# Kernel tuning notes

Measured on AMD Instinct MI355X. Metric: run time of the kernel, lower is better.

Reference implementation:

```python
import jax, jax.numpy as jnp
import numpy as np

N_NODES = 100000
N_EDGES = 600000
D = 128  # input_dim == output_dim (required by index_add into zeros_like(x) + residual)
EPS = 1e-5


def _linear_params(key, d_in, d_out):
    kw, kb = jax.random.split(key)
    bound = 1.0 / np.sqrt(d_in)
    w = jax.random.uniform(kw, (d_in, d_out), minval=-bound, maxval=bound, dtype=jnp.float32)
    b = jax.random.uniform(kb, (d_out,), minval=-bound, maxval=bound, dtype=jnp.float32)
    return w, b


def setup_inputs() -> dict:
    key = jax.random.key(0)
    ks = jax.random.split(key, 6)
    x = jax.random.normal(ks[0], (N_NODES, D), dtype=jnp.float32)
    edge_index = jax.random.randint(ks[1], (2, N_EDGES), 0, N_NODES, dtype=jnp.int32)
    w_m1, b_m1 = _linear_params(ks[2], 2 * D, D)
    w_m2, b_m2 = _linear_params(ks[3], D, D)
    w_u1, b_u1 = _linear_params(ks[4], 2 * D, D)
    w_u2, b_u2 = _linear_params(ks[5], D, D)
    gamma = jnp.ones((D,), dtype=jnp.float32)
    beta = jnp.zeros((D,), dtype=jnp.float32)
    return {
        "x": x, "edge_index": edge_index,
        "w_m1": w_m1, "b_m1": b_m1, "w_m2": w_m2, "b_m2": b_m2,
        "w_u1": w_u1, "b_u1": b_u1, "w_u2": w_u2, "b_u2": b_u2,
        "gamma": gamma, "beta": beta,
    }


def _layernorm(h, gamma, beta):
    mu = jnp.mean(h, axis=-1, keepdims=True)
    var = jnp.mean(jnp.square(h - mu), axis=-1, keepdims=True)
    return (h - mu) * jax.lax.rsqrt(var + EPS) * gamma + beta


def reference(x, edge_index, w_m1, b_m1, w_m2, b_m2, w_u1, b_u1, w_u2, b_u2, gamma, beta):
    row, col = edge_index[0], edge_index[1]
    # message MLP on concat of gathered endpoints: [E, 2D] -> [E, D]
    m_in = jnp.concatenate([x[row], x[col]], axis=-1)
    m = jax.nn.relu(m_in @ w_m1 + b_m1) @ w_m2 + b_m2
    # scatter-add messages to destination nodes (index_add along dim 0 with col)
    agg = jax.ops.segment_sum(m, col, num_segments=x.shape[0])
    # update MLP on [N, 2D] -> [N, D]
    u_in = jnp.concatenate([x, agg], axis=-1)
    h = jax.nn.relu(u_in @ w_u1 + b_u1) @ w_u2 + b_u2
    return _layernorm(h, gamma, beta) + x
```

## Files before the change

kernel.cpp:

```cpp
#include <hip/hip_runtime.h>
#include <hip/hip_bf16.h>
#include <stdint.h>

#define N_NODES 100000
#define N_EDGES 600000
#define D 128
#define EPS 1e-5f
#define SCAN_BS 512
#define ROW_MASK 0x1FFFF

#define PREP_BLOCKS 321
#define HIST_BLOCKS 2344
#define XF_BLOCKS   3125
#define SC_BLOCKS   2344
#define UPD_BLOCKS  3125

typedef __attribute__((ext_vector_type(8))) short short8;
typedef __attribute__((ext_vector_type(16))) float floatx16;


__device__ __forceinline__ uint32_t pack_bf16_rne(float lo, float hi) {
    uint32_t ul = __builtin_bit_cast(uint32_t, lo);
    uint32_t uh = __builtin_bit_cast(uint32_t, hi);
    ul += 0x7fffu + ((ul >> 16) & 1u);
    uh += 0x7fffu + ((uh >> 16) & 1u);
    return (ul >> 16) | (uh & 0xffff0000u);
}

__device__ __forceinline__ unsigned short f32_to_bf16_rne(float f) {
    uint32_t u = __builtin_bit_cast(uint32_t, f);
    u += 0x7fffu + ((u >> 16) & 1u);
    return (unsigned short)(u >> 16);
}

__device__ __forceinline__ float bflo(uint32_t a) { return __builtin_bit_cast(float, a << 16); }
__device__ __forceinline__ float bfhi(uint32_t a) { return __builtin_bit_cast(float, a & 0xffff0000u); }

__global__ void prep_hist(const float* __restrict__ w_m1, const float* __restrict__ w_u1,
                          const float* __restrict__ w_u2, const float* __restrict__ w_m2,
                          const float* __restrict__ b_m2,
                          unsigned short* __restrict__ wm1f, unsigned short* __restrict__ wu1tf,
                          unsigned short* __restrict__ wu2f, unsigned short* __restrict__ wcf,
                          float* __restrict__ vb,
                          const int* __restrict__ col, int* __restrict__ count,
                          int* __restrict__ rank) {
    if (blockIdx.x >= PREP_BLOCKS) {
        int e = (blockIdx.x - PREP_BLOCKS) * 256 + threadIdx.x;
        if (e < N_EDGES) rank[e] = atomicAdd(&count[col[e]], 1);
        return;
    }
    int idx = blockIdx.x * 256 + threadIdx.x;
    if (idx < 32768) {
        int j = idx & 7, lane = (idx >> 3) & 63, t = (idx >> 9) & 3, s = idx >> 11;
        int kk = s * 16 + ((lane >> 5) << 3) + j;
        wm1f[idx] = f32_to_bf16_rne(w_m1[kk * 128 + t * 32 + (lane & 31)]);
    } else if (idx < 49152) {
        int ii = idx - 32768;
        int j = ii & 7, lane = (ii >> 3) & 63, t = (ii >> 9) & 3, s = ii >> 11;
        int kk = s * 16 + ((lane >> 5) << 3) + j;
        wu1tf[ii] = f32_to_bf16_rne(w_u1[kk * 128 + t * 32 + (lane & 31)]);
    } else if (idx < 65536) {
        int ii = idx - 49152;
        int j = ii & 7, lane = (ii >> 3) & 63, t = (ii >> 9) & 3, s = ii >> 11;
        int kk = s * 16 + ((lane >> 5) << 3) + j;
        wu2f[ii] = f32_to_bf16_rne(w_u2[kk * 128 + t * 32 + (lane & 31)]);
    } else if (idx < 81920) {
        int ii = idx - 65536;
        int j = ii & 7, lane = (ii >> 3) & 63, t = (ii >> 9) & 3, s = ii >> 11;
        int kk = s * 16 + ((lane >> 5) << 3) + j;
        int nn = t * 32 + (lane & 31);
        float acc = 0.0f;
        for (int q = 0; q < 128; ++q)
            acc += w_m2[kk * 128 + q] * w_u1[(128 + q) * 128 + nn];
        wcf[ii] = f32_to_bf16_rne(acc);
    } else if (idx < 82048) {
        int nn = idx - 81920;
        float acc = 0.0f;
        for (int q = 0; q < 128; ++q)
            acc += b_m2[q] * w_u1[(128 + q) * 128 + nn];
        vb[nn] = acc;
    }
}

__global__ void scan_one(const int* __restrict__ count, int* __restrict__ base,
                         int* __restrict__ gcur) {
    __shared__ int tmp[SCAN_BS];
    __shared__ int bbase;
    int g = blockIdx.x * SCAN_BS + threadIdx.x;
    int v = (g < N_NODES) ? count[g] : 0;
    tmp[threadIdx.x] = v;
    __syncthreads();
    int acc = v;
#pragma unroll
    for (int off = 1; off < SCAN_BS; off <<= 1) {
        int add = (threadIdx.x >= off) ? tmp[threadIdx.x - off] : 0;
        __syncthreads();
        acc += add;
        tmp[threadIdx.x] = acc;
        __syncthreads();
    }
    if (threadIdx.x == SCAN_BS - 1) bbase = atomicAdd(gcur, acc);
    __syncthreads();
    if (g < N_NODES) base[g] = bbase + acc - v;
}

__launch_bounds__(64, 4)
__global__ void xform_scatter(const float* __restrict__ x, const short8* __restrict__ w1f,
                              const float* __restrict__ b1, unsigned short* __restrict__ xtb,
                              const int* __restrict__ row, const int* __restrict__ col,
                              const int* __restrict__ rank, const int* __restrict__ base,
                              int* __restrict__ srow) {
    if (blockIdx.x >= XF_BLOCKS) {
        int e4 = (((blockIdx.x - XF_BLOCKS) * 64 + threadIdx.x) << 2);
        if (e4 < N_EDGES) {
            int4 r4 = *(const int4*)(row + e4);
            int4 c4 = *(const int4*)(col + e4);
            int4 k4 = *(const int4*)(rank + e4);
            srow[base[c4.x] + k4.x] = r4.x | ((c4.x & 31) << 17);
            srow[base[c4.y] + k4.y] = r4.y | ((c4.y & 31) << 17);
            srow[base[c4.z] + k4.z] = r4.z | ((c4.z & 31) << 17);
            srow[base[c4.w] + k4.w] = r4.w | ((c4.w & 31) << 17);
        }
        return;
    }

    __shared__ __align__(16) short h1[32 * 136];
    const int lane = threadIdx.x;
    const int l31  = lane & 31;
    const int half = lane >> 5;
    short* hl = h1;

    const int nbase = blockIdx.x * 32;
    const int n = nbase + l31;
    const float* px = x + (size_t)n * D + half * 8;

    union { short8 v; uint32_t u[4]; } fa[8];
#pragma unroll
    for (int s = 0; s < 8; ++s) {
        const int off = s * 16;
        float4 a0 = *(const float4*)(px + off);
        float4 a1 = *(const float4*)(px + off + 4);
        fa[s].u[0] = pack_bf16_rne(a0.x, a0.y); fa[s].u[1] = pack_bf16_rne(a0.z, a0.w);
        fa[s].u[2] = pack_bf16_rne(a1.x, a1.y); fa[s].u[3] = pack_bf16_rne(a1.z, a1.w);
    }

#pragma unroll
    for (int p = 0; p < 2; ++p) {
        floatx16 acc[4];
#pragma unroll
        for (int t = 0; t < 4; ++t) acc[t] = (floatx16)0.0f;
#pragma unroll
        for (int s = 0; s < 8; ++s) {
#pragma unroll
            for (int t = 0; t < 4; ++t) {
                short8 wf = w1f[((p * 8 + s) * 4 + t) * 64 + lane];
                acc[t] = __builtin_amdgcn_mfma_f32_32x32x16_bf16(fa[s].v, wf, acc[t], 0, 0, 0);
            }
        }
#pragma unroll
        for (int t = 0; t < 4; ++t) {
            float bias = p ? b1[t * 32 + l31] : 0.0f;
#pragma unroll
            for (int r = 0; r < 16; ++r) {
                int m = (r & 3) + 8 * (r >> 2) + 4 * half;
                hl[m * 136 + t * 32 + l31] = (short)f32_to_bf16_rne(acc[t][r] + bias);
            }
        }
#pragma unroll
        for (int it = 0; it < 8; ++it) {
            int off = it * 512 + lane * 8;
            int r2 = off >> 7;
            int c2 = off & 127;
            short8 v = *(const short8*)(hl + r2 * 136 + c2);
            *(short8*)(xtb + (size_t)(nbase + r2) * 256 + p * 128 + c2) = v;
        }
    }
}

__launch_bounds__(64, 2)
__global__ void upd_kernel(const float* __restrict__ x, const uint32_t* __restrict__ xtb32,
                           const int* __restrict__ srowpk,
                           const int* __restrict__ base, const int* __restrict__ count,
                           const short8* __restrict__ wu1tf, const short8* __restrict__ wcf,
                           const short8* __restrict__ wu2f,
                           const float* __restrict__ b_u1, const float* __restrict__ vb,
                           const float* __restrict__ b_u2,
                           const float* __restrict__ gamma, const float* __restrict__ beta,
                           float* __restrict__ out) {
    __shared__ __align__(16) short h1[32 * 136];
    __shared__ __align__(16) uint32_t XBlds[32 * 64];
    const int lane = threadIdx.x;
    const int l31  = lane & 31;
    const int half = lane >> 5;
    const int t    = lane & 15;
    const int q16  = lane & 48;
    short* hl = h1;
    uint32_t* accu = (uint32_t*)hl;

    const int nbase = blockIdx.x * 32;
    const int nc = nbase + l31;

    const int b_l = base[nc];
    const int c_l = count[nc];
    const float dgv = (float)c_l;

    const int qsrc = q16 >> 1;
    const int qbeg = __shfl(b_l, qsrc);
    const int qend = __shfl(b_l, qsrc + 7) + __shfl(c_l, qsrc + 7);

    int ncm = (qend - qbeg + 15) >> 4;
    ncm = max(ncm, __shfl_xor(ncm, 16));
    ncm = max(ncm, __shfl_xor(ncm, 32));

#pragma unroll
    for (int i = 0; i < 8; ++i) {
        uint4 z; z.x = 0; z.y = 0; z.z = 0; z.w = 0;
        *((uint4*)accu + i * 64 + lane) = z;
    }

#pragma unroll
    for (int j = 0; j < 8; ++j) {
        int fi = j * 64 + lane;
        int i  = fi >> 4;
        int k  = fi & 15;
        uint4 v = *(const uint4*)(xtb32 + (size_t)(nbase + i) * 128 + 64 + (k << 2));
        *((uint4*)XBlds + fi) = v;
    }

    {
        float sl0 = 0.f, sl1 = 0.f, sl2 = 0.f, sl3 = 0.f;
        float sh0 = 0.f, sh1 = 0.f, sh2 = 0.f, sh3 = 0.f;
        int curnib = -1;

        auto flush = [&]() {
            uint4 o;
            o.x = pack_bf16_rne(sl0, sh0);
            o.y = pack_bf16_rne(sl1, sh1);
            o.z = pack_bf16_rne(sl2, sh2);
            o.w = pack_bf16_rne(sl3, sh3);
            *(uint4*)(accu + (curnib << 6) + (t << 2)) = o;
        };

        int pk = 0;
        { int idx = qbeg + t; if (idx < qend) pk = srowpk[idx]; }

        for (int c = 0; c < ncm; ++c) {
            const int rem = qend - qbeg - (c << 4);

            int pknext = 0;
            { int idx = qbeg + ((c + 1) << 4) + t; if (idx < qend) pknext = srowpk[idx]; }

            uint4 xt[16];
#pragma unroll
            for (int e = 0; e < 16; ++e) {
                int pv = __shfl(pk, q16 + e);
                uint4 z; z.x = 0; z.y = 0; z.z = 0; z.w = 0;
                xt[e] = z;
                if (e < rem)
                    xt[e] = *(const uint4*)(xtb32 + (size_t)(pv & ROW_MASK) * 128 + (t << 2));
            }

#pragma unroll
            for (int e = 0; e < 16; ++e) {
                int pv = __shfl(pk, q16 + e);
                if (e < rem) {
                    int nib = pv >> 17;
                    uint4 xb = *(const uint4*)(XBlds + (nib << 6) + (t << 2));
                    float a0 = fmaxf(bflo(xt[e].x) + bflo(xb.x), 0.f);
                    float b0 = fmaxf(bfhi(xt[e].x) + bfhi(xb.x), 0.f);
                    float a1 = fmaxf(bflo(xt[e].y) + bflo(xb.y), 0.f);
                    float b1 = fmaxf(bfhi(xt[e].y) + bfhi(xb.y), 0.f);
                    float a2 = fmaxf(bflo(xt[e].z) + bflo(xb.z), 0.f);
                    float b2 = fmaxf(bfhi(xt[e].z) + bfhi(xb.z), 0.f);
                    float a3 = fmaxf(bflo(xt[e].w) + bflo(xb.w), 0.f);
                    float b3 = fmaxf(bfhi(xt[e].w) + bfhi(xb.w), 0.f);
                    if (nib != curnib) {
                        if (curnib >= 0) flush();
                        curnib = nib;
                        sl0 = a0; sh0 = b0; sl1 = a1; sh1 = b1;
                        sl2 = a2; sh2 = b2; sl3 = a3; sh3 = b3;
                    } else {
                        sl0 += a0; sh0 += b0; sl1 += a1; sh1 += b1;
                        sl2 += a2; sh2 += b2; sl3 += a3; sh3 += b3;
                    }
                }
            }
            pk = pknext;
        }
        if (curnib >= 0) flush();
    }

    const float* px = x + (size_t)nc * D + half * 8;

    floatx16 acc[4];
#pragma unroll
    for (int tt = 0; tt < 4; ++tt) acc[tt] = (floatx16)0.0f;

#pragma unroll
    for (int s = 0; s < 16; ++s) {
        union { short8 v; uint32_t u[4]; } fa;
        const short8* bf;
        if (s < 8) {
            const int off = s * 16;
            float4 a0 = *(const float4*)(px + off);
            float4 a1 = *(const float4*)(px + off + 4);
            fa.u[0] = pack_bf16_rne(a0.x, a0.y); fa.u[1] = pack_bf16_rne(a0.z, a0.w);
            fa.u[2] = pack_bf16_rne(a1.x, a1.y); fa.u[3] = pack_bf16_rne(a1.z, a1.w);
            bf = wu1tf + (s * 4) * 64;
        } else {
            fa.v = *(const short8*)((const short*)accu + l31 * 128 + (s - 8) * 16 + half * 8);
            bf = wcf + ((s - 8) * 4) * 64;
        }
#pragma unroll
        for (int tt = 0; tt < 4; ++tt) {
            short8 wf = bf[tt * 64 + lane];
            acc[tt] = __builtin_amdgcn_mfma_f32_32x32x16_bf16(fa.v, wf, acc[tt], 0, 0, 0);
        }
    }

    float bu1[4], vbt[4];
#pragma unroll
    for (int tt = 0; tt < 4; ++tt) {
        bu1[tt] = b_u1[tt * 32 + l31];
        vbt[tt] = vb[tt * 32 + l31];
    }

#pragma unroll
    for (int r = 0; r < 16; ++r) {
        int m = (r & 3) + 8 * (r >> 2) + 4 * half;
        float dg = __shfl(dgv, m, 32);
#pragma unroll
        for (int tt = 0; tt < 4; ++tt) {
            float v = fmaxf(acc[tt][r] + bu1[tt] + dg * vbt[tt], 0.0f);
            hl[m * 136 + tt * 32 + l31] = (short)f32_to_bf16_rne(v);
        }
    }

    floatx16 acc2[4];
#pragma unroll
    for (int tt = 0; tt < 4; ++tt) acc2[tt] = (floatx16)0.0f;

#pragma unroll
    for (int s = 0; s < 8; ++s) {
        short8 af = *(const short8*)(hl + l31 * 136 + s * 16 + half * 8);
#pragma unroll
        for (int tt = 0; tt < 4; ++tt) {
            short8 wf = wu2f[(s * 4 + tt) * 64 + lane];
            acc2[tt] = __builtin_amdgcn_mfma_f32_32x32x16_bf16(af, wf, acc2[tt], 0, 0, 0);
        }
    }

    float g4[4], be4[4], bias2[4];
#pragma unroll
    for (int tt = 0; tt < 4; ++tt) {
        g4[tt]    = gamma[tt * 32 + l31];
        be4[tt]   = beta[tt * 32 + l31];
        bias2[tt] = b_u2[tt * 32 + l31];
    }

    float* hf = (float*)hl;
#pragma unroll
    for (int p = 0; p < 2; ++p) {
#pragma unroll
        for (int rr = 0; rr < 8; ++rr) {
            int r = p * 8 + rr;
            float hv[4];
            float s1 = 0.0f, s2 = 0.0f;
#pragma unroll
            for (int tt = 0; tt < 4; ++tt) {
                hv[tt] = acc2[tt][r] + bias2[tt];
                s1 += hv[tt];
                s2 += hv[tt] * hv[tt];
            }
#pragma unroll
            for (int mask = 1; mask < 32; mask <<= 1) {
                s1 += __shfl_xor(s1, mask);
                s2 += __shfl_xor(s2, mask);
            }
            float mean = s1 * (1.0f / 128.0f);
            float var  = s2 * (1.0f / 128.0f) - mean * mean;
            float rs   = rsqrtf(var + EPS);
            int m = (r & 3) + 8 * (r >> 2) + 4 * half;
            int mrow = m - 16 * p;
#pragma unroll
            for (int tt = 0; tt < 4; ++tt)
                hf[mrow * 132 + tt * 32 + l31] = (hv[tt] - mean) * rs * g4[tt] + be4[tt];
        }
#pragma unroll
        for (int it = 0; it < 8; ++it) {
            int qq = it * 64 + lane;
            int r2 = qq >> 5;
            int c4 = qq & 31;
            int node = nbase + 16 * p + r2;
            float4 v = *(const float4*)(hf + r2 * 132 + c4 * 4);
            float4 xr = *(const float4*)(x + (size_t)node * D + c4 * 4);
            v.x += xr.x; v.y += xr.y; v.z += xr.z; v.w += xr.w;
            *(float4*)(out + (size_t)node * D + c4 * 4) = v;
        }
    }
}

extern "C" void kernel_launch(void* const* d_in, const int* in_sizes, int n_in,
                              void* d_out, int out_size, void* d_ws, size_t ws_size,
                              hipStream_t stream) {
    const float* x     = (const float*)d_in[0];
    const int*   edge  = (const int*)d_in[1];
    const float* w_m1  = (const float*)d_in[2];
    const float* b_m1  = (const float*)d_in[3];
    const float* w_m2  = (const float*)d_in[4];
    const float* b_m2  = (const float*)d_in[5];
    const float* w_u1  = (const float*)d_in[6];
    const float* b_u1  = (const float*)d_in[7];
    const float* w_u2  = (const float*)d_in[8];
    const float* b_u2  = (const float*)d_in[9];
    const float* gamma = (const float*)d_in[10];
    const float* beta  = (const float*)d_in[11];
    float* out = (float*)d_out;

    char* ws = (char*)d_ws;
    size_t off = 0;
    auto alloc = [&](size_t bytes) { void* p = ws + off; off = (off + bytes + 15) & ~(size_t)15; return p; };

    unsigned short* xtb   = (unsigned short*)alloc((size_t)N_NODES * 256 * 2);
    unsigned short* wm1f  = (unsigned short*)alloc(256 * 128 * 2);
    unsigned short* wu1tf = (unsigned short*)alloc(128 * 128 * 2);
    unsigned short* wcf   = (unsigned short*)alloc(128 * 128 * 2);
    unsigned short* wu2f  = (unsigned short*)alloc(128 * 128 * 2);
    float* vb    = (float*)alloc(128 * 4);
    int* count   = (int*)alloc((size_t)N_NODES * 4 + 16);
    int* gcur    = count + N_NODES;
    int* base    = (int*)alloc((size_t)N_NODES * 4);
    int* rank    = (int*)alloc((size_t)N_EDGES * 4);
    int* srow    = (int*)alloc((size_t)N_EDGES * 4);

    const int* rowi = edge;
    const int* coli = edge + N_EDGES;
    const int NB = (N_NODES + SCAN_BS - 1) / SCAN_BS;

    (void)hipMemsetAsync(count, 0, (size_t)N_NODES * 4 + 16, stream);

    prep_hist<<<PREP_BLOCKS + HIST_BLOCKS, 256, 0, stream>>>(
        w_m1, w_u1, w_u2, w_m2, b_m2, wm1f, wu1tf, wu2f, wcf, vb, coli, count, rank);

    scan_one<<<NB, SCAN_BS, 0, stream>>>(count, base, gcur);

    xform_scatter<<<XF_BLOCKS + SC_BLOCKS, 64, 0, stream>>>(
        x, (const short8*)wm1f, b_m1, xtb, rowi, coli, rank, base, srow);

    upd_kernel<<<UPD_BLOCKS, 64, 0, stream>>>(
        x, (const uint32_t*)xtb, srow, base, count,
        (const short8*)wu1tf, (const short8*)wcf, (const short8*)wu2f,
        b_u1, vb, b_u2, gamma, beta, out);
}
```

Baseline: 256.3 us.

## Double-buffer edge-row gathers so loads overlap with the accumulate loop

Restructures the per-chunk gather loop into a two-stage software pipeline with A/B register buffers. The next chunk's 16 row loads are issued before the current chunk is consumed, and sched_barrier keeps the compiler from reordering them. Loads now happen unconditionally, with out-of-range entries clamped to row 0 and index reads clamped to N_EDGES-1, which removes the divergent guards. The aim is to hide global-memory gather latency behind compute, at the cost of roughly doubling the vector registers held for gathered rows, which may lower occupancy.

```diff
diff --git a/kernel.cpp b/kernel.cpp
--- a/kernel.cpp
+++ b/kernel.cpp
@@ -207,8 +207,9 @@
     const int qsrc = q16 >> 1;
     const int qbeg = __shfl(b_l, qsrc);
     const int qend = __shfl(b_l, qsrc + 7) + __shfl(c_l, qsrc + 7);
-
-    int ncm = (qend - qbeg + 15) >> 4;
+    const int rembase = qend - qbeg;
+
+    int ncm = (rembase + 15) >> 4;
     ncm = max(ncm, __shfl_xor(ncm, 16));
     ncm = max(ncm, __shfl_xor(ncm, 32));
 
@@ -241,30 +242,26 @@
             *(uint4*)(accu + (curnib << 6) + (t << 2)) = o;
         };
 
-        int pk = 0;
-        { int idx = qbeg + t; if (idx < qend) pk = srowpk[idx]; }
-
-        for (int c = 0; c < ncm; ++c) {
-            const int rem = qend - qbeg - (c << 4);
-
-            int pknext = 0;
-            { int idx = qbeg + ((c + 1) << 4) + t; if (idx < qend) pknext = srowpk[idx]; }
-
-            uint4 xt[16];
+        auto ldpk = [&](int c) -> int {
+            int idx = qbeg + (c << 4) + t;
+            return srowpk[min(idx, N_EDGES - 1)];
+        };
+
+        auto issue = [&](int pkv, int c, uint4* xt, int* pv) {
 #pragma unroll
             for (int e = 0; e < 16; ++e) {
-                int pv = __shfl(pk, q16 + e);
-                uint4 z; z.x = 0; z.y = 0; z.z = 0; z.w = 0;
-                xt[e] = z;
-                if (e < rem)
-                    xt[e] = *(const uint4*)(xtb32 + (size_t)(pv & ROW_MASK) * 128 + (t << 2));
-            }
-
+                int p = __shfl(pkv, q16 + e);
+                if ((c << 4) + e >= rembase) p = 0;
+                pv[e] = p;
+                xt[e] = *(const uint4*)(xtb32 + (size_t)(p & ROW_MASK) * 128 + (t << 2));
+            }
+        };
+
+        auto consume = [&](const uint4* xt, const int* pv, int rem) {
 #pragma unroll
             for (int e = 0; e < 16; ++e) {
-                int pv = __shfl(pk, q16 + e);
                 if (e < rem) {
-                    int nib = pv >> 17;
+                    int nib = pv[e] >> 17;
                     uint4 xb = *(const uint4*)(XBlds + (nib << 6) + (t << 2));
                     float a0 = fmaxf(bflo(xt[e].x) + bflo(xb.x), 0.f);
                     float b0 = fmaxf(bfhi(xt[e].x) + bfhi(xb.x), 0.f);
@@ -285,7 +282,25 @@
                     }
                 }
             }
-            pk = pknext;
+        };
+
+        uint4 xtA[16], xtB[16];
+        int pvA[16], pvB[16];
+
+        int pkc = ldpk(0);
+        issue(pkc, 0, xtA, pvA);
+        int pkn = ldpk(1);
+
+        for (int cc = 0; cc < ncm; cc += 2) {
+            issue(pkn, cc + 1, xtB, pvB);
+            pkc = ldpk(cc + 2);
+            __builtin_amdgcn_sched_barrier(0);
+            consume(xtA, pvA, rembase - (cc << 4));
+
+            issue(pkc, cc + 2, xtA, pvA);
+            pkn = ldpk(cc + 3);
+            __builtin_amdgcn_sched_barrier(0);
+            consume(xtB, pvB, rembase - ((cc + 1) << 4));
         }
         if (curnib >= 0) flush();
     }
```

After: 254.6 us. About the same (-0.7%).

## Pipeline edge-row gathers through LDS ring with async global_load_lds

Applied to the files above, without the earlier changes.

Replaces the register-held 16-edge gather batch in upd_kernel with a double-buffered LDS ring fed by global_load_lds, processing 4 edges per step and prefetching packed indices and gathered rows two steps ahead using manual vmcnt waits. It also raises launch bounds occupancy from 2 to 4 waves per SIMD hint. This aims to cut VGPR pressure and overlap gather latency with the accumulation work. The hand-tuned vmcnt counts are fragile, and smaller batches mean more loop iterations and synchronization overhead.

```diff
diff --git a/kernel.cpp b/kernel.cpp
--- a/kernel.cpp
+++ b/kernel.cpp
@@ -35,6 +35,17 @@
 
 __device__ __forceinline__ float bflo(uint32_t a) { return __builtin_bit_cast(float, a << 16); }
 __device__ __forceinline__ float bfhi(uint32_t a) { return __builtin_bit_cast(float, a & 0xffff0000u); }
+
+__device__ __forceinline__ void glds16(const void* g, void* l) {
+    __builtin_amdgcn_global_load_lds(
+        (const __attribute__((address_space(1))) void*)g,
+        (__attribute__((address_space(3))) void*)l, 16, 0, 0);
+}
+__device__ __forceinline__ void glds4(const void* g, void* l) {
+    __builtin_amdgcn_global_load_lds(
+        (const __attribute__((address_space(1))) void*)g,
+        (__attribute__((address_space(3))) void*)l, 4, 0, 0);
+}
 
 __global__ void prep_hist(const float* __restrict__ w_m1, const float* __restrict__ w_u1,
                           const float* __restrict__ w_u2, const float* __restrict__ w_m2,
@@ -177,7 +188,7 @@
     }
 }
 
-__launch_bounds__(64, 2)
+__launch_bounds__(64, 4)
 __global__ void upd_kernel(const float* __restrict__ x, const uint32_t* __restrict__ xtb32,
                            const int* __restrict__ srowpk,
                            const int* __restrict__ base, const int* __restrict__ count,
@@ -189,6 +200,8 @@
                            float* __restrict__ out) {
     __shared__ __align__(16) short h1[32 * 136];
     __shared__ __align__(16) uint32_t XBlds[32 * 64];
+    __shared__ __align__(16) uint32_t xtring[2048];
+    __shared__ __align__(16) uint32_t pkring[128];
     const int lane = threadIdx.x;
     const int l31  = lane & 31;
     const int half = lane >> 5;
@@ -207,8 +220,9 @@
     const int qsrc = q16 >> 1;
     const int qbeg = __shfl(b_l, qsrc);
     const int qend = __shfl(b_l, qsrc + 7) + __shfl(c_l, qsrc + 7);
-
-    int ncm = (qend - qbeg + 15) >> 4;
+    const int rembase = qend - qbeg;
+
+    int ncm = (rembase + 3) >> 2;
     ncm = max(ncm, __shfl_xor(ncm, 16));
     ncm = max(ncm, __shfl_xor(ncm, 32));
 
@@ -227,10 +241,11 @@
         *((uint4*)XBlds + fi) = v;
     }
 
-    {
+    if (ncm > 0) {
         float sl0 = 0.f, sl1 = 0.f, sl2 = 0.f, sl3 = 0.f;
         float sh0 = 0.f, sh1 = 0.f, sh2 = 0.f, sh3 = 0.f;
         int curnib = -1;
+        int pkcur = 0, pknext = 0;
 
         auto flush = [&]() {
             uint4 o;
@@ -241,39 +256,37 @@
             *(uint4*)(accu + (curnib << 6) + (t << 2)) = o;
         };
 
-        int pk = 0;
-        { int idx = qbeg + t; if (idx < qend) pk = srowpk[idx]; }
-
-        for (int c = 0; c < ncm; ++c) {
-            const int rem = qend - qbeg - (c << 4);
-
-            int pknext = 0;
-            { int idx = qbeg + ((c + 1) << 4) + t; if (idx < qend) pknext = srowpk[idx]; }
-
-            uint4 xt[16];
-#pragma unroll
-            for (int e = 0; e < 16; ++e) {
-                int pv = __shfl(pk, q16 + e);
-                uint4 z; z.x = 0; z.y = 0; z.z = 0; z.w = 0;
-                xt[e] = z;
-                if (e < rem)
-                    xt[e] = *(const uint4*)(xtb32 + (size_t)(pv & ROW_MASK) * 128 + (t << 2));
-            }
-
-#pragma unroll
-            for (int e = 0; e < 16; ++e) {
-                int pv = __shfl(pk, q16 + e);
+        auto stage_pk = [&](int c, int slot) {
+            int idx = qbeg + (c << 2) + (t & 3);
+            glds4(srowpk + min(idx, N_EDGES - 1), &pkring[slot * 64]);
+        };
+
+        auto stage_xt = [&](int pkv, int slot) {
+#pragma unroll
+            for (int j = 0; j < 4; ++j) {
+                int pj = __shfl(pkv, q16 + j);
+                const uint32_t* g = xtb32 + (size_t)(pj & ROW_MASK) * 128 + (t << 2);
+                glds16(g, &xtring[slot * 1024 + j * 256]);
+            }
+        };
+
+        auto consume = [&](int c) {
+            const int rem = rembase - (c << 2);
+            const uint32_t* ring = xtring + ((c & 1) << 10);
+#pragma unroll
+            for (int e = 0; e < 4; ++e) {
                 if (e < rem) {
-                    int nib = pv >> 17;
+                    int nib = __shfl(pkcur, q16 + e) >> 17;
+                    uint4 xt = *(const uint4*)(ring + (e << 8) + (lane << 2));
                     uint4 xb = *(const uint4*)(XBlds + (nib << 6) + (t << 2));
-                    float a0 = fmaxf(bflo(xt[e].x) + bflo(xb.x), 0.f);
-                    float b0 = fmaxf(bfhi(xt[e].x) + bfhi(xb.x), 0.f);
-                    float a1 = fmaxf(bflo(xt[e].y) + bflo(xb.y), 0.f);
-                    float b1 = fmaxf(bfhi(xt[e].y) + bfhi(xb.y), 0.f);
-                    float a2 = fmaxf(bflo(xt[e].z) + bflo(xb.z), 0.f);
-                    float b2 = fmaxf(bfhi(xt[e].z) + bfhi(xb.z), 0.f);
-                    float a3 = fmaxf(bflo(xt[e].w) + bflo(xb.w), 0.f);
-                    float b3 = fmaxf(bfhi(xt[e].w) + bfhi(xb.w), 0.f);
+                    float a0 = fmaxf(bflo(xt.x) + bflo(xb.x), 0.f);
+                    float b0 = fmaxf(bfhi(xt.x) + bfhi(xb.x), 0.f);
+                    float a1 = fmaxf(bflo(xt.y) + bflo(xb.y), 0.f);
+                    float b1 = fmaxf(bfhi(xt.y) + bfhi(xb.y), 0.f);
+                    float a2 = fmaxf(bflo(xt.z) + bflo(xb.z), 0.f);
+                    float b2 = fmaxf(bfhi(xt.z) + bfhi(xb.z), 0.f);
+                    float a3 = fmaxf(bflo(xt.w) + bflo(xb.w), 0.f);
+                    float b3 = fmaxf(bfhi(xt.w) + bfhi(xb.w), 0.f);
                     if (nib != curnib) {
                         if (curnib >= 0) flush();
                         curnib = nib;
@@ -285,7 +298,29 @@
                     }
                 }
             }
-            pk = pknext;
+        };
+
+        asm volatile("s_waitcnt vmcnt(0)" ::: "memory");
+
+        stage_pk(0, 0);
+        stage_pk(1, 1);
+        asm volatile("s_waitcnt vmcnt(1)" ::: "memory");
+        pkcur = (int)pkring[lane];
+        stage_xt(pkcur, 0);
+        asm volatile("s_waitcnt vmcnt(4)" ::: "memory");
+        pknext = (int)pkring[64 + lane];
+        stage_pk(2, 0);
+        stage_xt(pknext, 1);
+
+        for (int c = 0; c < ncm; ++c) {
+            asm volatile("s_waitcnt vmcnt(5)" ::: "memory");
+            __builtin_amdgcn_sched_barrier(0);
+            consume(c);
+            asm volatile("s_waitcnt vmcnt(4)" ::: "memory");
+            pkcur = pknext;
+            pknext = (int)pkring[(c & 1) * 64 + lane];
+            stage_pk(c + 3, (c + 1) & 1);
+            stage_xt(pknext, c & 1);
         }
         if (curnib >= 0) flush();
     }
```

Measured after the change: 279.8 us. +9.2%, slower.

## Split edge aggregation into separate fine-grained kernel writing aggregates in place

Applied to the files above, without the earlier changes.

Moves the gather/ReLU/segment-sum edge aggregation out of the update kernel into a new agg_kernel that handles 8 nodes per block across many more blocks. It processes edges in chunks of 8 with all loads issued ahead of the math. The bf16 aggregates overwrite the column-transform half of the xtb buffer in place, and the slimmer update kernel reads them from global memory for its MFMA stage. The aim is better occupancy and load balance for the irregular, latency-bound gather. The cost is an extra launch plus an extra global round trip of the aggregate buffer.

```diff
diff --git a/kernel.cpp b/kernel.cpp
--- a/kernel.cpp
+++ b/kernel.cpp
@@ -13,6 +13,7 @@
 #define HIST_BLOCKS 2344
 #define XF_BLOCKS   3125
 #define SC_BLOCKS   2344
+#define AGG_BLOCKS  12500
 #define UPD_BLOCKS  3125
 
 typedef __attribute__((ext_vector_type(8))) short short8;
@@ -177,54 +178,38 @@
     }
 }
 
-__launch_bounds__(64, 2)
-__global__ void upd_kernel(const float* __restrict__ x, const uint32_t* __restrict__ xtb32,
-                           const int* __restrict__ srowpk,
-                           const int* __restrict__ base, const int* __restrict__ count,
-                           const short8* __restrict__ wu1tf, const short8* __restrict__ wcf,
-                           const short8* __restrict__ wu2f,
-                           const float* __restrict__ b_u1, const float* __restrict__ vb,
-                           const float* __restrict__ b_u2,
-                           const float* __restrict__ gamma, const float* __restrict__ beta,
-                           float* __restrict__ out) {
-    __shared__ __align__(16) short h1[32 * 136];
-    __shared__ __align__(16) uint32_t XBlds[32 * 64];
+__launch_bounds__(64, 4)
+__global__ void agg_kernel(uint32_t* __restrict__ xtb32, const int* __restrict__ srowpk,
+                           const int* __restrict__ base, const int* __restrict__ count) {
+    __shared__ __align__(16) uint32_t accu[8 * 64];
+    __shared__ __align__(16) uint32_t XBl[8 * 64];
     const int lane = threadIdx.x;
-    const int l31  = lane & 31;
-    const int half = lane >> 5;
     const int t    = lane & 15;
     const int q16  = lane & 48;
-    short* hl = h1;
-    uint32_t* accu = (uint32_t*)hl;
-
-    const int nbase = blockIdx.x * 32;
-    const int nc = nbase + l31;
-
-    const int b_l = base[nc];
-    const int c_l = count[nc];
-    const float dgv = (float)c_l;
-
-    const int qsrc = q16 >> 1;
+
+    const int nbase = blockIdx.x * 8;
+
+    const int b_l = base[nbase + (lane & 7)];
+    const int c_l = count[nbase + (lane & 7)];
+    const int qsrc = q16 >> 3;
     const int qbeg = __shfl(b_l, qsrc);
-    const int qend = __shfl(b_l, qsrc + 7) + __shfl(c_l, qsrc + 7);
-
-    int ncm = (qend - qbeg + 15) >> 4;
+    const int qend = __shfl(b_l, qsrc + 1) + __shfl(c_l, qsrc + 1);
+    const int rembase = qend - qbeg;
+
+    int ncm = (rembase + 7) >> 3;
     ncm = max(ncm, __shfl_xor(ncm, 16));
     ncm = max(ncm, __shfl_xor(ncm, 32));
 
-#pragma unroll
-    for (int i = 0; i < 8; ++i) {
+    {
         uint4 z; z.x = 0; z.y = 0; z.z = 0; z.w = 0;
-        *((uint4*)accu + i * 64 + lane) = z;
-    }
-
-#pragma unroll
-    for (int j = 0; j < 8; ++j) {
-        int fi = j * 64 + lane;
-        int i  = fi >> 4;
-        int k  = fi & 15;
-        uint4 v = *(const uint4*)(xtb32 + (size_t)(nbase + i) * 128 + 64 + (k << 2));
-        *((uint4*)XBlds + fi) = v;
+        *((uint4*)accu + lane) = z;
+        *((uint4*)accu + 64 + lane) = z;
+    }
+#pragma unroll
+    for (int it = 0; it < 2; ++it) {
+        int fi4 = it * 64 + lane;
+        int i = fi4 >> 4, k4 = fi4 & 15;
+        *((uint4*)XBl + fi4) = *(const uint4*)(xtb32 + (size_t)(nbase + i) * 128 + 64 + (k4 << 2));
     }
 
     {
@@ -241,31 +226,25 @@
             *(uint4*)(accu + (curnib << 6) + (t << 2)) = o;
         };
 
-        int pk = 0;
-        { int idx = qbeg + t; if (idx < qend) pk = srowpk[idx]; }
-
         for (int c = 0; c < ncm; ++c) {
-            const int rem = qend - qbeg - (c << 4);
-
-            int pknext = 0;
-            { int idx = qbeg + ((c + 1) << 4) + t; if (idx < qend) pknext = srowpk[idx]; }
-
-            uint4 xt[16];
-#pragma unroll
-            for (int e = 0; e < 16; ++e) {
-                int pv = __shfl(pk, q16 + e);
-                uint4 z; z.x = 0; z.y = 0; z.z = 0; z.w = 0;
-                xt[e] = z;
-                if (e < rem)
-                    xt[e] = *(const uint4*)(xtb32 + (size_t)(pv & ROW_MASK) * 128 + (t << 2));
-            }
-
-#pragma unroll
-            for (int e = 0; e < 16; ++e) {
-                int pv = __shfl(pk, q16 + e);
+            int idx = qbeg + (c << 3) + (t & 7);
+            int pk = srowpk[min(idx, N_EDGES - 1)];
+            const int rem = rembase - (c << 3);
+
+            uint4 xt[8]; int pv[8];
+#pragma unroll
+            for (int e = 0; e < 8; ++e) {
+                int p = __shfl(pk, q16 + e);
+                if (e >= rem) p = 0;
+                pv[e] = p;
+                xt[e] = *(const uint4*)(xtb32 + (size_t)(p & ROW_MASK) * 128 + (t << 2));
+            }
+            __builtin_amdgcn_sched_barrier(0);
+#pragma unroll
+            for (int e = 0; e < 8; ++e) {
                 if (e < rem) {
-                    int nib = pv >> 17;
-                    uint4 xb = *(const uint4*)(XBlds + (nib << 6) + (t << 2));
+                    int nib = (pv[e] >> 17) & 7;
+                    uint4 xb = *(const uint4*)(XBl + (nib << 6) + (t << 2));
                     float a0 = fmaxf(bflo(xt[e].x) + bflo(xb.x), 0.f);
                     float b0 = fmaxf(bfhi(xt[e].x) + bfhi(xb.x), 0.f);
                     float a1 = fmaxf(bflo(xt[e].y) + bflo(xb.y), 0.f);
@@ -285,12 +264,39 @@
                     }
                 }
             }
-            pk = pknext;
         }
         if (curnib >= 0) flush();
     }
 
+#pragma unroll
+    for (int it = 0; it < 2; ++it) {
+        int fi4 = it * 64 + lane;
+        int i = fi4 >> 4, k4 = fi4 & 15;
+        *(uint4*)(xtb32 + (size_t)(nbase + i) * 128 + 64 + (k4 << 2)) = *((uint4*)accu + fi4);
+    }
+}
+
+__launch_bounds__(64, 4)
+__global__ void upd_kernel(const float* __restrict__ x, const uint32_t* __restrict__ xtb32,
+                           const int* __restrict__ count,
+                           const short8* __restrict__ wu1tf, const short8* __restrict__ wcf,
+                           const short8* __restrict__ wu2f,
+                           const float* __restrict__ b_u1, const float* __restrict__ vb,
+                           const float* __restrict__ b_u2,
+                           const float* __restrict__ gamma, const float* __restrict__ beta,
+                           float* __restrict__ out) {
+    __shared__ __align__(16) short h1[32 * 136];
+    const int lane = threadIdx.x;
+    const int l31  = lane & 31;
+    const int half = lane >> 5;
+    short* hl = h1;
+
+    const int nbase = blockIdx.x * 32;
+    const int nc = nbase + l31;
+    const float dgv = (float)count[nc];
+
     const float* px = x + (size_t)nc * D + half * 8;
+    const short* xtbs = (const short*)xtb32;
 
     floatx16 acc[4];
 #pragma unroll
@@ -308,7 +314,7 @@
             fa.u[2] = pack_bf16_rne(a1.x, a1.y); fa.u[3] = pack_bf16_rne(a1.z, a1.w);
             bf = wu1tf + (s * 4) * 64;
         } else {
-            fa.v = *(const short8*)((const short*)accu + l31 * 128 + (s - 8) * 16 + half * 8);
+            fa.v = *(const short8*)(xtbs + (size_t)nc * 256 + 128 + (s - 8) * 16 + half * 8);
             bf = wcf + ((s - 8) * 4) * 64;
         }
 #pragma unroll
@@ -447,8 +453,11 @@
     xform_scatter<<<XF_BLOCKS + SC_BLOCKS, 64, 0, stream>>>(
         x, (const short8*)wm1f, b_m1, xtb, rowi, coli, rank, base, srow);
 
+    agg_kernel<<<AGG_BLOCKS, 64, 0, stream>>>(
+        (uint32_t*)xtb, srow, base, count);
+
     upd_kernel<<<UPD_BLOCKS, 64, 0, stream>>>(
-        x, (const uint32_t*)xtb, srow, base, count,
+        x, (const uint32_t*)xtb, count,
         (const short8*)wu1tf, (const short8*)wcf, (const short8*)wu2f,
         b_u1, vb, b_u2, gamma, beta, out);
 }
```

After: 257.1 us. No clear change (+0.3%).
